# Kernel optimization log

Hardware: AMD Instinct MI355X
Metric: run time of the kernel (lower is better)

## Reference

```python
import jax, jax.numpy as jnp
import numpy as np

K = 3
STRIDE = 1
PAD = 1


def _conv2d(x, w, b):
    y = jax.lax.conv_general_dilated(
        x, w, window_strides=(STRIDE, STRIDE),
        padding=[(PAD, PAD), (PAD, PAD)],
        dimension_numbers=("NCHW", "OIHW", "NCHW"))
    return y + b[None, :, None, None]


def _bilinear_sample(xb, py, px):
    # xb: [C, H, W]; py, px: [K2, Ho, Wo] float sample coords
    C, H, W = xb.shape
    y0 = jnp.floor(py)
    x0 = jnp.floor(px)
    ay = py - y0  # frac weights
    ax = px - x0
    out = jnp.zeros((C,) + py.shape, dtype=xb.dtype)
    corners = [
        (y0, x0, (1.0 - ay) * (1.0 - ax)),
        (y0, x0 + 1.0, (1.0 - ay) * ax),
        (y0 + 1.0, x0, ay * (1.0 - ax)),
        (y0 + 1.0, x0 + 1.0, ay * ax),
    ]
    for yc, xc, wgt in corners:
        valid = (yc >= 0) & (yc < H) & (xc >= 0) & (xc < W)
        yi = jnp.clip(yc, 0, H - 1).astype(jnp.int32)
        xi = jnp.clip(xc, 0, W - 1).astype(jnp.int32)
        g = xb[:, yi, xi]  # [C, K2, Ho, Wo]
        out = out + g * (wgt * valid.astype(xb.dtype))[None]
    return out


def _deform_forward(x, weight, bias, p_weight, p_bias):
    B, Cin, H, W = x.shape
    Cout = weight.shape[0]
    K2 = K * K
    # offset / mask prediction conv
    pout = _conv2d(x, p_weight, p_bias)  # [B, 3*K2, Ho, Wo]
    o1, o2, m = jnp.split(pout, 3, axis=1)
    offset = jnp.concatenate([o1, o2], axis=1)  # [B, 2*K2, Ho, Wo]
    mask = jax.nn.sigmoid(m)  # [B, K2, Ho, Wo]
    Ho, Wo = mask.shape[2], mask.shape[3]
    # torchvision layout: channel 2k = dy_k, 2k+1 = dx_k
    off = offset.reshape(B, K2, 2, Ho, Wo)
    dy, dx = off[:, :, 0], off[:, :, 1]  # [B, K2, Ho, Wo]
    ki = (jnp.arange(K2) // K).astype(x.dtype)  # kernel row
    kj = (jnp.arange(K2) % K).astype(x.dtype)   # kernel col
    base_y = jnp.arange(Ho, dtype=x.dtype) * STRIDE - PAD  # [Ho]
    base_x = jnp.arange(Wo, dtype=x.dtype) * STRIDE - PAD  # [Wo]
    py = base_y[None, None, :, None] + ki[None, :, None, None] + dy
    px = base_x[None, None, None, :] + kj[None, :, None, None] + dx
    sampled = jax.vmap(_bilinear_sample)(x, py, px)  # [B, Cin, K2, Ho, Wo]
    sampled = sampled * mask[:, None]
    w = weight.reshape(Cout, Cin, K2)
    out = jnp.einsum('bckhw,ock->bohw', sampled, w) + bias[None, :, None, None]
    return out


def setup_inputs() -> dict:
    key = jax.random.key(0)
    k1, k2, k3 = jax.random.split(key, 3)
    B, Cin, Cout, H, W = 4, 256, 256, 64, 64
    x = jax.random.normal(k1, (B, Cin, H, W), dtype=jnp.float32)
    fan_in = Cin * K * K
    weight = jax.random.normal(k2, (Cout, Cin, K, K), dtype=jnp.float32) / np.sqrt(fan_in)
    bias = jnp.zeros((Cout,), dtype=jnp.float32)
    # small random offset/mask predictor (zero-init in the original; randomized
    # here so the deformable sampling path is exercised)
    p_weight = jax.random.normal(k3, (3 * K * K, Cin, K, K), dtype=jnp.float32) * 0.02
    p_bias = jnp.zeros((3 * K * K,), dtype=jnp.float32)
    return {"x": x, "weight": weight, "bias": bias, "p_weight": p_weight, "p_bias": p_bias}


def reference(x, weight, bias, p_weight, p_bias):
    return _deform_forward(x, weight, bias, p_weight, p_bias)
```

## Files before the change

kernel.cpp:

```cpp
#include <hip/hip_runtime.h>
#include <stdint.h>


#define CIN 256
#define COUT 256
#define HWS 4096
#define MTOT 16384
#define KTOT 2304
#define SPLITK 8

typedef __attribute__((ext_vector_type(8))) short bf16x8;
typedef __attribute__((ext_vector_type(4))) float f32x4;

__device__ __forceinline__ unsigned short f2bf(float f) {
  unsigned int u = __float_as_uint(f);
  unsigned int r = (u + 0x7fffu + ((u >> 16) & 1u)) >> 16;
  return (unsigned short)r;
}
__device__ __forceinline__ float bf2f(unsigned short u) {
  return __uint_as_float(((unsigned int)u) << 16);
}
__device__ __forceinline__ float bflo(unsigned int u) { return __uint_as_float(u << 16); }
__device__ __forceinline__ float bfhi(unsigned int u) { return __uint_as_float(u & 0xffff0000u); }

__device__ __forceinline__ void gload_lds16(const void* g, void* l) {
  __builtin_amdgcn_global_load_lds((const __attribute__((address_space(1))) void*)g,
                                   (__attribute__((address_space(3))) void*)l, 16, 0, 0);
}

#define GLOAD16(D, P) asm volatile("global_load_dwordx4 %0, %1, off" : "=v"(D) : "v"(P))
#define WAITVM(N)                                            \
  {                                                          \
    asm volatile("s_waitcnt vmcnt(" #N ")" ::: "memory");    \
    __builtin_amdgcn_sched_barrier(0);                       \
  }
#define BARRIER_LGKM                                                  \
  { asm volatile("s_waitcnt lgkmcnt(0)\n\ts_barrier" ::: "memory"); }

#define ASW(c, rr) ((c) ^ (((rr) & 7) << 3))

__global__ __launch_bounds__(256) void prep_and_transpose(const float* __restrict__ x,
                                                          const float* __restrict__ w,
                                                          const float* __restrict__ pw,
                                                          unsigned short* __restrict__ xt,
                                                          unsigned short* __restrict__ WB,
                                                          unsigned short* __restrict__ PWs,
                                                          unsigned short* __restrict__ zerop) {
  __shared__ float tile[32][33];
  int bid = blockIdx.x;
  if (bid < 4096) {
    int b = bid >> 10;
    int rest = bid & 1023;
    int hw0 = (rest & 127) * 32;
    int c0 = ((rest >> 7) & 7) * 32;
    int tx = threadIdx.x & 31, ty = threadIdx.x >> 5;
    for (int i = ty; i < 32; i += 8)
      tile[i][tx] = x[(size_t)(b * CIN + c0 + i) * HWS + hw0 + tx];
    __syncthreads();
    for (int r = ty; r < 32; r += 8)
      xt[(size_t)(b * HWS + hw0 + r) * CIN + c0 + tx] = f2bf(tile[tx][r]);
  } else {
    int idx = (bid - 4096) * 256 + threadIdx.x;
    if (idx < 512)
      *(uint4*)(zerop + idx * 8) = make_uint4(0, 0, 0, 0);
    if (idx < KTOT * COUT) {
      int f = idx;
      int e = f & 7;
      int row = (f >> 3) & 15;
      int quad = (f >> 7) & 3;
      int j = (f >> 9) & 15;
      int t = f >> 13;
      int kk = t * 32 + quad * 8 + e;
      int o = j * 16 + row;
      int k = kk >> 8, c = kk & 255;
      WB[f] = f2bf(w[o * KTOT + c * 9 + k]);
    } else {
      int f2 = idx - KTOT * COUT;
      int t_ = f2 & 7;
      int rest = f2 >> 3;
      int j = rest & 31;
      int kk = (rest >> 5) * 8 + t_;
      int k = kk >> 8, c = kk & 255;
      float v = (j < 27) ? pw[j * KTOT + c * 9 + k] : 0.0f;
      PWs[f2] = f2bf(v);
    }
  }
}

__global__ __launch_bounds__(256) void offset_conv_sk(const unsigned short* __restrict__ xt,
                                                      const unsigned short* __restrict__ PWs,
                                                      const unsigned short* __restrict__ zerop,
                                                      float* __restrict__ Pbuf) {
  __shared__ unsigned short Al[64 * 32];
  __shared__ unsigned short Bl[1024];
  int tid = threadIdx.x;
  int lane = tid & 63, wv = tid >> 6;
  int mt = (blockIdx.x & 7) * 32 + (blockIdx.x >> 3);
  int m0 = mt * 64;
  int s = blockIdx.y;
  int b = m0 >> 12;
  int hw0 = m0 & 4095;
  f32x4 acc[2] = {};

  for (int tt = 0; tt < 72 / SPLITK; ++tt) {
    int t = s * (72 / SPLITK) + tt;
    int k = t >> 3, c0 = (t & 7) * 32;
    int dyk = k / 3 - 1;
    int dxk = k % 3 - 1;
    __syncthreads();
    if (tid < 128)
      gload_lds16(PWs + (size_t)t * 1024 + tid * 8, &Bl[tid * 8]);
    {
      int r = tid >> 2;
      int hw = hw0 + r;
      int h = hw >> 6, wwp = hw & 63;
      int y = h + dyk, xx = wwp + dxk;
      bool valid = ((unsigned)y < 64u) && ((unsigned)xx < 64u);
      const unsigned short* src = valid
          ? xt + ((size_t)((b << 12) + (y << 6) + xx) << 8) + c0 + (tid & 3) * 8
          : zerop;
      gload_lds16(src, &Al[tid * 8]);
    }
    __syncthreads();
    int row = lane & 15, quad = lane >> 4;
    bf16x8 af = *(const bf16x8*)&Al[(wv * 16 + row) * 32 + quad * 8];
    for (int j = 0; j < 2; ++j) {
      bf16x8 bfr = *(const bf16x8*)&Bl[(quad * 32 + j * 16 + row) * 8];
      acc[j] = __builtin_amdgcn_mfma_f32_16x16x32_bf16(af, bfr, acc[j], 0, 0, 0);
    }
  }

  int row = lane & 15, quad = lane >> 4;
  for (int j = 0; j < 2; ++j) {
    int n = j * 16 + row;
    for (int r_ = 0; r_ < 4; ++r_) {
      int m = m0 + wv * 16 + quad * 4 + r_;
      Pbuf[((size_t)s * MTOT + m) * 32 + n] = acc[j][r_];
    }
  }
}

__device__ __forceinline__ void bilin8p(const uint4 c00, const uint4 c01,
                                        const uint4 c10, const uint4 c11,
                                        const float4 w4, unsigned short* dst) {
  uint4 o;
  float v0, v1;
  v0 = w4.x * bflo(c00.x) + w4.y * bflo(c01.x) + w4.z * bflo(c10.x) + w4.w * bflo(c11.x);
  v1 = w4.x * bfhi(c00.x) + w4.y * bfhi(c01.x) + w4.z * bfhi(c10.x) + w4.w * bfhi(c11.x);
  o.x = (unsigned)f2bf(v0) | ((unsigned)f2bf(v1) << 16);
  v0 = w4.x * bflo(c00.y) + w4.y * bflo(c01.y) + w4.z * bflo(c10.y) + w4.w * bflo(c11.y);
  v1 = w4.x * bfhi(c00.y) + w4.y * bfhi(c01.y) + w4.z * bfhi(c10.y) + w4.w * bfhi(c11.y);
  o.y = (unsigned)f2bf(v0) | ((unsigned)f2bf(v1) << 16);
  v0 = w4.x * bflo(c00.z) + w4.y * bflo(c01.z) + w4.z * bflo(c10.z) + w4.w * bflo(c11.z);
  v1 = w4.x * bfhi(c00.z) + w4.y * bfhi(c01.z) + w4.z * bfhi(c10.z) + w4.w * bfhi(c11.z);
  o.z = (unsigned)f2bf(v0) | ((unsigned)f2bf(v1) << 16);
  v0 = w4.x * bflo(c00.w) + w4.y * bflo(c01.w) + w4.z * bflo(c10.w) + w4.w * bflo(c11.w);
  v1 = w4.x * bfhi(c00.w) + w4.y * bfhi(c01.w) + w4.z * bfhi(c10.w) + w4.w * bfhi(c11.w);
  o.w = (unsigned)f2bf(v0) | ((unsigned)f2bf(v1) << 16);
  *(uint4*)dst = o;
}

#define MFMA16P(B0, B1, B2, B3)                                                          \
  acc[0][0] = __builtin_amdgcn_mfma_f32_16x16x32_bf16(afr0, B0, acc[0][0], 0, 0, 0);     \
  acc[0][1] = __builtin_amdgcn_mfma_f32_16x16x32_bf16(afr0, B1, acc[0][1], 0, 0, 0);     \
  acc[1][0] = __builtin_amdgcn_mfma_f32_16x16x32_bf16(afr1, B0, acc[1][0], 0, 0, 0);     \
  acc[1][1] = __builtin_amdgcn_mfma_f32_16x16x32_bf16(afr1, B1, acc[1][1], 0, 0, 0);     \
  acc[2][0] = __builtin_amdgcn_mfma_f32_16x16x32_bf16(afr2, B0, acc[2][0], 0, 0, 0);     \
  acc[2][1] = __builtin_amdgcn_mfma_f32_16x16x32_bf16(afr2, B1, acc[2][1], 0, 0, 0);     \
  acc[3][0] = __builtin_amdgcn_mfma_f32_16x16x32_bf16(afr3, B0, acc[3][0], 0, 0, 0);     \
  acc[3][1] = __builtin_amdgcn_mfma_f32_16x16x32_bf16(afr3, B1, acc[3][1], 0, 0, 0);     \
  acc[0][0] = __builtin_amdgcn_mfma_f32_16x16x32_bf16(afr4, B2, acc[0][0], 0, 0, 0);     \
  acc[0][1] = __builtin_amdgcn_mfma_f32_16x16x32_bf16(afr4, B3, acc[0][1], 0, 0, 0);     \
  acc[1][0] = __builtin_amdgcn_mfma_f32_16x16x32_bf16(afr5, B2, acc[1][0], 0, 0, 0);     \
  acc[1][1] = __builtin_amdgcn_mfma_f32_16x16x32_bf16(afr5, B3, acc[1][1], 0, 0, 0);     \
  acc[2][0] = __builtin_amdgcn_mfma_f32_16x16x32_bf16(afr6, B2, acc[2][0], 0, 0, 0);     \
  acc[2][1] = __builtin_amdgcn_mfma_f32_16x16x32_bf16(afr6, B3, acc[2][1], 0, 0, 0);     \
  acc[3][0] = __builtin_amdgcn_mfma_f32_16x16x32_bf16(afr7, B2, acc[3][0], 0, 0, 0);     \
  acc[3][1] = __builtin_amdgcn_mfma_f32_16x16x32_bf16(afr7, B3, acc[3][1], 0, 0, 0);

#define FITER_P2(P, PAR, GI0, GI1, GI2, GI3, GC0, GC1, GC2, GC3,                         \
                 BC0, BC1, BC2, BC3, BI0, BI1, BI2, BI3)                                 \
  {                                                                                      \
    const unsigned short* btn = bpb + (size_t)(2 * ((P) + 1)) * 8192;                    \
    GLOAD16(BI0, btn);                                                                   \
    GLOAD16(BI1, btn + 512);                                                             \
    GLOAD16(BI2, btn + 8192);                                                            \
    GLOAD16(BI3, btn + 8192 + 512);                                                      \
    if ((((P) + 2) & 3) == 0) dI4 = Tbl[r][((P) + 2) >> 2][0];                           \
    int cb = ((2 * (P) + 4) & 7) * 32 + qo8;                                             \
    GLOAD16(GI0, xtb + dI4.x + cb);                                                      \
    GLOAD16(GI1, xtb + dI4.y + cb);                                                      \
    GLOAD16(GI2, xtb + dI4.z + cb);                                                      \
    GLOAD16(GI3, xtb + dI4.w + cb);                                                      \
    afr0 = *(const bf16x8*)&As[PAR][row][ASW(quad * 8, row)];                            \
    afr1 = *(const bf16x8*)&As[PAR][16 + row][ASW(quad * 8, row)];                       \
    afr2 = *(const bf16x8*)&As[PAR][32 + row][ASW(quad * 8, row)];                       \
    afr3 = *(const bf16x8*)&As[PAR][48 + row][ASW(quad * 8, row)];                       \
    afr4 = *(const bf16x8*)&As[PAR][row][ASW(32 + quad * 8, row)];                       \
    afr5 = *(const bf16x8*)&As[PAR][16 + row][ASW(32 + quad * 8, row)];                  \
    afr6 = *(const bf16x8*)&As[PAR][32 + row][ASW(32 + quad * 8, row)];                  \
    afr7 = *(const bf16x8*)&As[PAR][48 + row][ASW(32 + quad * 8, row)];                  \
    if ((((P) + 1) & 3) == 0) dW4 = *(float4*)&Tbl[r][((P) + 1) >> 2][1];                \
    WAITVM(12)                                                                           \
    MFMA16P(BC0, BC1, BC2, BC3)                                                          \
    WAITVM(8)                                                                            \
    bilin8p(GC0, GC1, GC2, GC3, dW4, &As[PAR ^ 1][r][ASW(qo8, r)]);                      \
    BARRIER_LGKM                                                                         \
  }

__global__ __launch_bounds__(512, 2) void fused_gemm(const unsigned short* __restrict__ xt,
                                                     const float* __restrict__ Pbuf,
                                                     const float* __restrict__ p_bias,
                                                     const unsigned short* __restrict__ WB,
                                                     const float* __restrict__ bias,
                                                     float* __restrict__ out) {
  __shared__ unsigned short As[2][64][64];
  __shared__ int4 Tbl[64][9][2];

  int tid = threadIdx.x;
  int lane = tid & 63, wv = tid >> 6;
  int mt = (blockIdx.x & 7) * 32 + (blockIdx.x >> 3);
  int mb = mt * 64;
  int b = mb >> 12;
  int hw0 = mb & 4095;
  const unsigned short* xtb = xt + ((size_t)b << 20);

  for (int pr = tid; pr < 576; pr += 512) {
    int lm = pr / 9;
    int k = pr - lm * 9;
    int m = mb + lm;

    float dy = p_bias[2 * k];
    float dx = p_bias[2 * k + 1];
    float mv = p_bias[18 + k];
#pragma unroll
    for (int s = 0; s < SPLITK; ++s) {
      const float* p = Pbuf + ((size_t)s * MTOT + m) * 32;
      dy += p[2 * k];
      dx += p[2 * k + 1];
      mv += p[18 + k];
    }
    float mk = 1.0f / (1.0f + __expf(-mv));

    int hw = m & 4095, h = hw >> 6, ww = hw & 63;
    float py = (float)(h - 1 + k / 3) + dy;
    float px = (float)(ww - 1 + k % 3) + dx;
    float y0f = floorf(py), x0f = floorf(px);
    float ay = py - y0f, ax = px - x0f;
    int y0 = (int)y0f, x0 = (int)x0f;

    float w00 = (1.f - ay) * (1.f - ax) * mk;
    float w01 = (1.f - ay) * ax * mk;
    float w10 = ay * (1.f - ax) * mk;
    float w11 = ay * ax * mk;

    float vy0 = ((unsigned)y0 < 64u) ? 1.f : 0.f;
    float vy1 = ((unsigned)(y0 + 1) < 64u) ? 1.f : 0.f;
    float vx0 = ((unsigned)x0 < 64u) ? 1.f : 0.f;
    float vx1 = ((unsigned)(x0 + 1) < 64u) ? 1.f : 0.f;
    w00 *= vy0 * vx0; w01 *= vy0 * vx1; w10 *= vy1 * vx0; w11 *= vy1 * vx1;

    int yc0 = min(max(y0, 0), 63), yc1 = min(max(y0 + 1, 0), 63);
    int xc0 = min(max(x0, 0), 63), xc1 = min(max(x0 + 1, 0), 63);

    Tbl[lm][k][0] = make_int4((yc0 * 64 + xc0) * 256, (yc0 * 64 + xc1) * 256,
                              (yc1 * 64 + xc0) * 256, (yc1 * 64 + xc1) * 256);
    *(float4*)&Tbl[lm][k][1] = make_float4(w00, w01, w10, w11);
  }
  __syncthreads();

  int r = tid >> 3;
  int qo8 = (tid & 7) * 8;

  int4 dI4 = Tbl[r][0][0];
  float4 dW4 = *(float4*)&Tbl[r][0][1];

  int row = lane & 15, quad = lane >> 4;
  const unsigned short* bpb = WB + (size_t)(wv * 2) * 512 + quad * 128 + row * 8;

  f32x4 acc[4][2] = {};
  uint4 gA0, gA1, gA2, gA3;
  uint4 gB0, gB1, gB2, gB3;
  bf16x8 bA0, bA1, bA2, bA3;
  bf16x8 bB0, bB1, bB2, bB3;
  bf16x8 afr0, afr1, afr2, afr3, afr4, afr5, afr6, afr7;

  {
    uint4 p00 = *(const uint4*)(xtb + dI4.x + qo8);
    uint4 p01 = *(const uint4*)(xtb + dI4.y + qo8);
    uint4 p10 = *(const uint4*)(xtb + dI4.z + qo8);
    uint4 p11 = *(const uint4*)(xtb + dI4.w + qo8);
    bilin8p(p00, p01, p10, p11, dW4, &As[0][r][ASW(qo8, r)]);
    GLOAD16(bA0, bpb);
    GLOAD16(bA1, bpb + 512);
    GLOAD16(bA2, bpb + 8192);
    GLOAD16(bA3, bpb + 8192 + 512);
    int cb1 = 64 + qo8;
    GLOAD16(gA0, xtb + dI4.x + cb1);
    GLOAD16(gA1, xtb + dI4.y + cb1);
    GLOAD16(gA2, xtb + dI4.z + cb1);
    GLOAD16(gA3, xtb + dI4.w + cb1);
  }
  BARRIER_LGKM

#pragma unroll 1
  for (int p = 0; p < 34; p += 2) {
    FITER_P2(p,     0, gB0, gB1, gB2, gB3, gA0, gA1, gA2, gA3,
                       bA0, bA1, bA2, bA3, bB0, bB1, bB2, bB3)
    FITER_P2(p + 1, 1, gA0, gA1, gA2, gA3, gB0, gB1, gB2, gB3,
                       bB0, bB1, bB2, bB3, bA0, bA1, bA2, bA3)
  }

  {
    const unsigned short* btn = bpb + (size_t)70 * 8192;
    GLOAD16(bB0, btn);
    GLOAD16(bB1, btn + 512);
    GLOAD16(bB2, btn + 8192);
    GLOAD16(bB3, btn + 8192 + 512);
    afr0 = *(const bf16x8*)&As[0][row][ASW(quad * 8, row)];
    afr1 = *(const bf16x8*)&As[0][16 + row][ASW(quad * 8, row)];
    afr2 = *(const bf16x8*)&As[0][32 + row][ASW(quad * 8, row)];
    afr3 = *(const bf16x8*)&As[0][48 + row][ASW(quad * 8, row)];
    afr4 = *(const bf16x8*)&As[0][row][ASW(32 + quad * 8, row)];
    afr5 = *(const bf16x8*)&As[0][16 + row][ASW(32 + quad * 8, row)];
    afr6 = *(const bf16x8*)&As[0][32 + row][ASW(32 + quad * 8, row)];
    afr7 = *(const bf16x8*)&As[0][48 + row][ASW(32 + quad * 8, row)];
    WAITVM(8)
    MFMA16P(bA0, bA1, bA2, bA3)
    WAITVM(4)
    bilin8p(gA0, gA1, gA2, gA3, dW4, &As[1][r][ASW(qo8, r)]);
    BARRIER_LGKM
  }
  {
    afr0 = *(const bf16x8*)&As[1][row][ASW(quad * 8, row)];
    afr1 = *(const bf16x8*)&As[1][16 + row][ASW(quad * 8, row)];
    afr2 = *(const bf16x8*)&As[1][32 + row][ASW(quad * 8, row)];
    afr3 = *(const bf16x8*)&As[1][48 + row][ASW(quad * 8, row)];
    afr4 = *(const bf16x8*)&As[1][row][ASW(32 + quad * 8, row)];
    afr5 = *(const bf16x8*)&As[1][16 + row][ASW(32 + quad * 8, row)];
    afr6 = *(const bf16x8*)&As[1][32 + row][ASW(32 + quad * 8, row)];
    afr7 = *(const bf16x8*)&As[1][48 + row][ASW(32 + quad * 8, row)];
    WAITVM(0)
    MFMA16P(bB0, bB1, bB2, bB3)
  }

#pragma unroll
  for (int j = 0; j < 2; ++j) {
    int o = wv * 32 + j * 16 + row;
    float bo = bias[o];
#pragma unroll
    for (int i = 0; i < 4; ++i) {
      int hw = hw0 + i * 16 + quad * 4;
      float4 v;
      v.x = acc[i][j][0] + bo;
      v.y = acc[i][j][1] + bo;
      v.z = acc[i][j][2] + bo;
      v.w = acc[i][j][3] + bo;
      *(float4*)(out + (((size_t)(b * COUT + o)) << 12) + hw) = v;
    }
  }
}

extern "C" void kernel_launch(void* const* d_in, const int* in_sizes, int n_in,
                              void* d_out, int out_size, void* d_ws, size_t ws_size,
                              hipStream_t stream) {
  const float* x        = (const float*)d_in[0];
  const float* weight   = (const float*)d_in[1];
  const float* bias     = (const float*)d_in[2];
  const float* p_weight = (const float*)d_in[3];
  const float* p_bias   = (const float*)d_in[4];
  float* out = (float*)d_out;
  char* ws = (char*)d_ws;

  const size_t OFF_XT   = 0;
  const size_t OFF_WB   = OFF_XT + 8388608;
  const size_t OFF_PW   = OFF_WB + 1179648;
  const size_t OFF_P    = OFF_PW + 147456;
  const size_t OFF_ZP   = OFF_P + 16777216;

  unsigned short* xt    = (unsigned short*)(ws + OFF_XT);
  unsigned short* WB    = (unsigned short*)(ws + OFF_WB);
  unsigned short* PWs   = (unsigned short*)(ws + OFF_PW);
  float* Pbuf           = (float*)(ws + OFF_P);
  unsigned short* zerop = (unsigned short*)(ws + OFF_ZP);

  prep_and_transpose<<<4096 + 2592, 256, 0, stream>>>(x, weight, p_weight, xt, WB, PWs, zerop);
  offset_conv_sk<<<dim3(MTOT / 64, SPLITK), 256, 0, stream>>>(xt, PWs, zerop, Pbuf);
  fused_gemm<<<256, 512, 0, stream>>>(xt, Pbuf, p_bias, WB, bias, out);
}
```

Measured before the change: 127.0 us.

## Fuse offset-prediction conv into main deformable GEMM kernel

Removes the separate split-K offset conv kernel and its global partial-sum buffer. Each fused_gemm block now computes its own 64-row offset/mask tile with MFMA, one K-slice per wave, and reduces the partials across waves in shared memory before building the bilinear table. This avoids a launch and a large global write/read of partials. The cost is a serialized prologue in each block and much more LDS, which may limit occupancy.

```diff
diff --git a/kernel.cpp b/kernel.cpp
--- a/kernel.cpp
+++ b/kernel.cpp
@@ -87,59 +87,6 @@
   }
 }
 
-__global__ __launch_bounds__(256) void offset_conv_sk(const unsigned short* __restrict__ xt,
-                                                      const unsigned short* __restrict__ PWs,
-                                                      const unsigned short* __restrict__ zerop,
-                                                      float* __restrict__ Pbuf) {
-  __shared__ unsigned short Al[64 * 32];
-  __shared__ unsigned short Bl[1024];
-  int tid = threadIdx.x;
-  int lane = tid & 63, wv = tid >> 6;
-  int mt = (blockIdx.x & 7) * 32 + (blockIdx.x >> 3);
-  int m0 = mt * 64;
-  int s = blockIdx.y;
-  int b = m0 >> 12;
-  int hw0 = m0 & 4095;
-  f32x4 acc[2] = {};
-
-  for (int tt = 0; tt < 72 / SPLITK; ++tt) {
-    int t = s * (72 / SPLITK) + tt;
-    int k = t >> 3, c0 = (t & 7) * 32;
-    int dyk = k / 3 - 1;
-    int dxk = k % 3 - 1;
-    __syncthreads();
-    if (tid < 128)
-      gload_lds16(PWs + (size_t)t * 1024 + tid * 8, &Bl[tid * 8]);
-    {
-      int r = tid >> 2;
-      int hw = hw0 + r;
-      int h = hw >> 6, wwp = hw & 63;
-      int y = h + dyk, xx = wwp + dxk;
-      bool valid = ((unsigned)y < 64u) && ((unsigned)xx < 64u);
-      const unsigned short* src = valid
-          ? xt + ((size_t)((b << 12) + (y << 6) + xx) << 8) + c0 + (tid & 3) * 8
-          : zerop;
-      gload_lds16(src, &Al[tid * 8]);
-    }
-    __syncthreads();
-    int row = lane & 15, quad = lane >> 4;
-    bf16x8 af = *(const bf16x8*)&Al[(wv * 16 + row) * 32 + quad * 8];
-    for (int j = 0; j < 2; ++j) {
-      bf16x8 bfr = *(const bf16x8*)&Bl[(quad * 32 + j * 16 + row) * 8];
-      acc[j] = __builtin_amdgcn_mfma_f32_16x16x32_bf16(af, bfr, acc[j], 0, 0, 0);
-    }
-  }
-
-  int row = lane & 15, quad = lane >> 4;
-  for (int j = 0; j < 2; ++j) {
-    int n = j * 16 + row;
-    for (int r_ = 0; r_ < 4; ++r_) {
-      int m = m0 + wv * 16 + quad * 4 + r_;
-      Pbuf[((size_t)s * MTOT + m) * 32 + n] = acc[j][r_];
-    }
-  }
-}
-
 __device__ __forceinline__ void bilin8p(const uint4 c00, const uint4 c01,
                                         const uint4 c10, const uint4 c11,
                                         const float4 w4, unsigned short* dst) {
@@ -209,37 +156,72 @@
   }
 
 __global__ __launch_bounds__(512, 2) void fused_gemm(const unsigned short* __restrict__ xt,
-                                                     const float* __restrict__ Pbuf,
+                                                     const unsigned short* __restrict__ PWs,
                                                      const float* __restrict__ p_bias,
                                                      const unsigned short* __restrict__ WB,
                                                      const float* __restrict__ bias,
                                                      float* __restrict__ out) {
   __shared__ unsigned short As[2][64][64];
   __shared__ int4 Tbl[64][9][2];
+  __shared__ float Ptl[8][64][32];
 
   int tid = threadIdx.x;
   int lane = tid & 63, wv = tid >> 6;
+  int row = lane & 15, quad = lane >> 4;
   int mt = (blockIdx.x & 7) * 32 + (blockIdx.x >> 3);
   int mb = mt * 64;
   int b = mb >> 12;
   int hw0 = mb & 4095;
   const unsigned short* xtb = xt + ((size_t)b << 20);
 
+  {
+    f32x4 aco[4][2] = {};
+    for (int tt = 0; tt < 9; ++tt) {
+      int t = wv * 9 + tt;
+      int k = t >> 3, c0 = (t & 7) * 32;
+      int dyk = k / 3 - 1, dxk = k % 3 - 1;
+      const unsigned short* pb = PWs + (size_t)t * 1024 + (quad * 32 + row) * 8;
+      bf16x8 ob0 = *(const bf16x8*)pb;
+      bf16x8 ob1 = *(const bf16x8*)(pb + 128);
+#pragma unroll
+      for (int rs = 0; rs < 4; ++rs) {
+        int hw = hw0 + rs * 16 + row;
+        int h = hw >> 6, wq = hw & 63;
+        int y = h + dyk, xx = wq + dxk;
+        bf16x8 oa = {};
+        if (((unsigned)y < 64u) && ((unsigned)xx < 64u))
+          oa = *(const bf16x8*)(xtb + (size_t)(((y << 6) + xx) << 8) + c0 + quad * 8);
+        aco[rs][0] = __builtin_amdgcn_mfma_f32_16x16x32_bf16(oa, ob0, aco[rs][0], 0, 0, 0);
+        aco[rs][1] = __builtin_amdgcn_mfma_f32_16x16x32_bf16(oa, ob1, aco[rs][1], 0, 0, 0);
+      }
+    }
+#pragma unroll
+    for (int rs = 0; rs < 4; ++rs)
+#pragma unroll
+      for (int j = 0; j < 2; ++j)
+#pragma unroll
+        for (int e = 0; e < 4; ++e)
+          Ptl[wv][rs * 16 + quad * 4 + e][j * 16 + row] = aco[rs][j][e];
+  }
+  __syncthreads();
+
+  for (int i = tid; i < 2048; i += 512) {
+    int lm = i >> 5, n = i & 31;
+    float s = Ptl[0][lm][n];
+#pragma unroll
+    for (int w = 1; w < 8; ++w) s += Ptl[w][lm][n];
+    Ptl[0][lm][n] = s;
+  }
+  __syncthreads();
+
   for (int pr = tid; pr < 576; pr += 512) {
     int lm = pr / 9;
     int k = pr - lm * 9;
     int m = mb + lm;
 
-    float dy = p_bias[2 * k];
-    float dx = p_bias[2 * k + 1];
-    float mv = p_bias[18 + k];
-#pragma unroll
-    for (int s = 0; s < SPLITK; ++s) {
-      const float* p = Pbuf + ((size_t)s * MTOT + m) * 32;
-      dy += p[2 * k];
-      dx += p[2 * k + 1];
-      mv += p[18 + k];
-    }
+    float dy = p_bias[2 * k] + Ptl[0][lm][2 * k];
+    float dx = p_bias[2 * k + 1] + Ptl[0][lm][2 * k + 1];
+    float mv = p_bias[18 + k] + Ptl[0][lm][18 + k];
     float mk = 1.0f / (1.0f + __expf(-mv));
 
     int hw = m & 4095, h = hw >> 6, ww = hw & 63;
@@ -275,7 +257,6 @@
   int4 dI4 = Tbl[r][0][0];
   float4 dW4 = *(float4*)&Tbl[r][0][1];
 
-  int row = lane & 15, quad = lane >> 4;
   const unsigned short* bpb = WB + (size_t)(wv * 2) * 512 + quad * 128 + row * 8;
 
   f32x4 acc[4][2] = {};
@@ -375,16 +356,13 @@
   const size_t OFF_XT   = 0;
   const size_t OFF_WB   = OFF_XT + 8388608;
   const size_t OFF_PW   = OFF_WB + 1179648;
-  const size_t OFF_P    = OFF_PW + 147456;
-  const size_t OFF_ZP   = OFF_P + 16777216;
+  const size_t OFF_ZP   = OFF_PW + 147456;
 
   unsigned short* xt    = (unsigned short*)(ws + OFF_XT);
   unsigned short* WB    = (unsigned short*)(ws + OFF_WB);
   unsigned short* PWs   = (unsigned short*)(ws + OFF_PW);
-  float* Pbuf           = (float*)(ws + OFF_P);
   unsigned short* zerop = (unsigned short*)(ws + OFF_ZP);
 
   prep_and_transpose<<<4096 + 2592, 256, 0, stream>>>(x, weight, p_weight, xt, WB, PWs, zerop);
-  offset_conv_sk<<<dim3(MTOT / 64, SPLITK), 256, 0, stream>>>(xt, PWs, zerop, Pbuf);
-  fused_gemm<<<256, 512, 0, stream>>>(xt, Pbuf, p_bias, WB, bias, out);
-}
+  fused_gemm<<<256, 512, 0, stream>>>(xt, PWs, p_bias, WB, bias, out);
+}
```

Result: no change. 125.7 us (-1.0%).
